# Kernel tuning notes

Hardware: AMD Instinct MI355X
Metric: run time of the kernel (lower is better)

## Reference

```python
import jax, jax.numpy as jnp
import numpy as np

B_GRAPHS = 16
N_PER_GRAPH = 128
N_NODES = B_GRAPHS * N_PER_GRAPH  # 2048
HIDDEN = 256
N_HEADS = 8
HEAD_DIM = HIDDEN // N_HEADS
N_LAYERS = 4
K_RPE = 4
N_EDGES = 32768
NUM_NODE_FEATS = 32
NUM_EDGE_TYPES = 16
MAX_DEGREE = 100
MLP_HID = HIDDEN // 2


def _layernorm(x, s, b):
    m = x.mean(-1, keepdims=True)
    v = jnp.var(x, axis=-1, keepdims=True)
    return (x - m) / jnp.sqrt(v + 1e-5) * s + b


def setup_inputs() -> dict:
    key = jax.random.key(0)
    ks = jax.random.split(key, 24)
    s = 0.02
    x_idx = jax.random.randint(ks[0], (N_NODES,), 0, NUM_NODE_FEATS)
    # edges are intra-graph (the torch code drops cross-graph edges)
    src = jax.random.randint(ks[1], (N_EDGES,), 0, N_NODES)
    dst = (src // N_PER_GRAPH) * N_PER_GRAPH + jax.random.randint(ks[2], (N_EDGES,), 0, N_PER_GRAPH)
    edge_index = jnp.stack([src, dst])
    edge_attr = jax.random.randint(ks[3], (N_EDGES,), 0, NUM_EDGE_TYPES)
    batch = jnp.repeat(jnp.arange(B_GRAPHS), N_PER_GRAPH)
    L = N_LAYERS
    return {
        'x_idx': x_idx, 'edge_index': edge_index, 'edge_attr': edge_attr, 'batch': batch,
        'node_emb': jax.random.normal(ks[4], (NUM_NODE_FEATS, HIDDEN)) * s,
        'edge_emb': jax.random.normal(ks[5], (NUM_EDGE_TYPES, N_HEADS)) * s,
        'degree_emb': jax.random.normal(ks[6], (MAX_DEGREE + 1, HIDDEN)) * s,
        'rpe_W1': jax.random.normal(ks[7], (K_RPE + 1, MLP_HID)) * s,
        'rpe_b1': jnp.zeros((MLP_HID,)),
        'rpe_W2': jax.random.normal(ks[8], (MLP_HID, N_HEADS)) * s,
        'rpe_b2': jnp.zeros((N_HEADS,)),
        'Wq': jax.random.normal(ks[9], (L, HIDDEN, HIDDEN)) * s, 'bq': jnp.zeros((L, HIDDEN)),
        'Wk': jax.random.normal(ks[10], (L, HIDDEN, HIDDEN)) * s, 'bk': jnp.zeros((L, HIDDEN)),
        'Wv': jax.random.normal(ks[11], (L, HIDDEN, HIDDEN)) * s, 'bv': jnp.zeros((L, HIDDEN)),
        'Wo': jax.random.normal(ks[12], (L, HIDDEN, HIDDEN)) * s, 'bo': jnp.zeros((L, HIDDEN)),
        'ln1_s': jnp.ones((L, HIDDEN)), 'ln1_b': jnp.zeros((L, HIDDEN)),
        'ln2_s': jnp.ones((L, HIDDEN)), 'ln2_b': jnp.zeros((L, HIDDEN)),
        'ff_W1': jax.random.normal(ks[13], (L, HIDDEN, 2 * HIDDEN)) * s, 'ff_b1': jnp.zeros((L, 2 * HIDDEN)),
        'ff_W2': jax.random.normal(ks[14], (L, 2 * HIDDEN, HIDDEN)) * s, 'ff_b2': jnp.zeros((L, HIDDEN)),
    }


def _forward(x_idx, edge_index, edge_attr, batch,
             node_emb, edge_emb, degree_emb, rpe_W1, rpe_b1, rpe_W2, rpe_b2,
             Wq, bq, Wk, bk, Wv, bv, Wo, bo, ln1_s, ln1_b, ln2_s, ln2_b,
             ff_W1, ff_b1, ff_W2, ff_b2):
    B, n, H, N = B_GRAPHS, N_PER_GRAPH, N_HEADS, N_NODES
    x = node_emb[x_idx]                               # [N, d]
    src, dst = edge_index[0], edge_index[1]
    # degrees from source endpoints (scatter_add in torch)
    deg = jnp.zeros((N,), jnp.int32).at[src].add(1)
    deg_c = jnp.minimum(deg, MAX_DEGREE)

    # ---- RRWP + edge-type attention bias, block-diagonal over graphs ----
    g = batch[src]
    intra = (batch[src] == batch[dst])                # torch code skips cross-graph edges
    u = src % n
    v = dst % n
    intra_f = intra.astype(jnp.float32)
    inv_du = intra_f / jnp.maximum(deg[src], 1).astype(jnp.float32)
    inv_dv = intra_f / jnp.maximum(deg[dst], 1).astype(jnp.float32)
    # random-walk transition matrix per graph [B, n, n]
    T = (jnp.zeros((B, n, n), jnp.float32)
         .at[g, u, v].add(inv_du)
         .at[g, v, u].add(inv_dv))
    # symmetric edge-type bias per graph [B, n, n, H]
    ev = edge_emb[edge_attr] * intra_f[:, None]
    EB = (jnp.zeros((B, n, n, H), jnp.float32)
          .at[g, u, v].add(ev)
          .at[g, v, u].add(ev))
    # walk powers I, T, T^2, ..., T^K -> [B, n, n, K+1]
    I = jnp.broadcast_to(jnp.eye(n, dtype=jnp.float32), (B, n, n))
    powers = [I, T]
    cur = T
    for _ in range(2, K_RPE + 1):
        cur = cur @ T
        powers.append(cur)
    walk = jnp.stack(powers, axis=-1)
    pair = jax.nn.relu(walk @ rpe_W1 + rpe_b1) @ rpe_W2 + rpe_b2   # [B, n, n, H]
    block = (pair + EB).transpose(0, 3, 1, 2)                      # [B, H, n, n]
    ib = jnp.arange(B)
    full = jnp.full((H, B, n, B, n), -jnp.inf, jnp.float32)
    full = full.at[:, ib, :, ib, :].set(block)                     # diag blocks
    attn_bias = full.reshape(H, N, N)

    # ---- transformer stack ----
    deg_vec = degree_emb[deg_c]
    scale = 1.0 / jnp.sqrt(jnp.float32(HEAD_DIM))
    for l in range(N_LAYERS):
        x = x + deg_vec
        Q = (x @ Wq[l] + bq[l]).reshape(N, H, HEAD_DIM)
        K_ = (x @ Wk[l] + bk[l]).reshape(N, H, HEAD_DIM)
        V = (x @ Wv[l] + bv[l]).reshape(N, H, HEAD_DIM)
        scores = jnp.einsum('ihd,jhd->hij', Q, K_) * scale + attn_bias
        aw = jax.nn.softmax(scores, axis=-1)
        out = jnp.einsum('hij,jhd->ihd', aw, V).reshape(N, HIDDEN)
        out = out @ Wo[l] + bo[l]
        x = _layernorm(x + out, ln1_s[l], ln1_b[l])
        ff = jax.nn.relu(x @ ff_W1[l] + ff_b1[l]) @ ff_W2[l] + ff_b2[l]
        x = _layernorm(x + ff, ln2_s[l], ln2_b[l])
    # global add pool
    return jax.ops.segment_sum(x, batch, num_segments=B)


def reference(x_idx, edge_index, edge_attr, batch,
              node_emb, edge_emb, degree_emb, rpe_W1, rpe_b1, rpe_W2, rpe_b2,
              Wq, bq, Wk, bk, Wv, bv, Wo, bo, ln1_s, ln1_b, ln2_s, ln2_b,
              ff_W1, ff_b1, ff_W2, ff_b2):
    return _forward(x_idx, edge_index, edge_attr, batch,
                    node_emb, edge_emb, degree_emb, rpe_W1, rpe_b1, rpe_W2, rpe_b2,
                    Wq, bq, Wk, bk, Wv, bv, Wo, bo, ln1_s, ln1_b, ln2_s, ln2_b,
                    ff_W1, ff_b1, ff_W2, ff_b2)
```

## Files before the change

kernel.cpp:

```cpp
#include <hip/hip_runtime.h>
#include <hip/hip_bf16.h>

#define B_GRAPHS 16
#define NPG 128
#define NN 2048
#define HIDDEN 256
#define N_HEADS 8
#define HEAD_DIM 32
#define N_LAYERS 4
#define N_EDGES 32768
#define MLP_HID 128
#define MAX_DEG 100

typedef __hip_bfloat16 bf16;
typedef unsigned short ushort_t;
typedef __attribute__((ext_vector_type(8))) short short8;
typedef __attribute__((ext_vector_type(4))) float f32x4;

__device__ __forceinline__ float us2f(ushort_t u) {
    return __uint_as_float(((unsigned)u) << 16);
}
__device__ __forceinline__ ushort_t f2us(float f) {
    unsigned u = __float_as_uint(f);
    return (ushort_t)((u + 0x7FFFu + ((u >> 16) & 1u)) >> 16);
}
__device__ __forceinline__ bool is_bf16_mode(const unsigned* probe) {
    return probe[0] != 0x3F800000u;
}
#define MFMA16(a, b, c) __builtin_amdgcn_mfma_f32_16x16x32_bf16(a, b, c, 0, 0, 0)

__device__ __forceinline__ void gload_lds16(const void* g, void* l) {
    __builtin_amdgcn_global_load_lds(
        (const __attribute__((address_space(1))) unsigned int*)g,
        (__attribute__((address_space(3))) unsigned int*)l, 16, 0, 0);
}
#define SBAR __builtin_amdgcn_s_barrier()
#define WAITPIPE asm volatile("s_waitcnt vmcnt(16) lgkmcnt(0)" ::: "memory")
#define WAITLAST asm volatile("s_waitcnt vmcnt(0) lgkmcnt(0)" ::: "memory")
#define LBAR do { asm volatile("s_waitcnt lgkmcnt(0)" ::: "memory"); SBAR; \
                  asm volatile("" ::: "memory"); } while (0)

#define NW 23
__device__ const int c_wsizes[NW] = {
    8192, 128, 25856, 640, 128, 1024, 8,
    262144, 1024, 262144, 1024, 262144, 1024, 262144, 1024,
    1024, 1024, 1024, 1024,
    524288, 2048, 524288, 1024};
#define TOTW 2144392

#define OFF_NODE_EMB 0
#define OFF_EDGE_EMB 8192
#define OFF_DEG_EMB  8320
#define OFF_RPE_W1   34176
#define OFF_RPE_B1   34816
#define OFF_RPE_W2   34944
#define OFF_RPE_B2   35968
#define OFF_BO       1087624
#define OFF_LN1S     1088648
#define OFF_LN1B     1089672
#define OFF_LN2S     1090696
#define OFF_LN2B     1091720
#define OFF_FFB1     1617032
#define OFF_FFB2     2143368

#define WB_QKV 0
#define WB_O   786432
#define WB_F1  1048576
#define WB_F2  1572864
#define WB_TOT 2097152
#define QKVB_TOT 3072

struct SrcPtrs { const void* p[NW]; };

__global__ void convert_kernel(SrcPtrs sp, const unsigned* __restrict__ probe,
                               float* __restrict__ Wc, float* __restrict__ qkvb) {
    int i = blockIdx.x * 256 + threadIdx.x;
    bool isbf = is_bf16_mode(probe);
    auto rd = [&](int seg, int off) -> float {
        return isbf ? us2f(((const ushort_t*)sp.p[seg])[off])
                    : ((const float*)sp.p[seg])[off];
    };
    if (i < TOTW) {
        int seg = 0, off = i;
        while (seg < NW - 1 && off >= c_wsizes[seg]) { off -= c_wsizes[seg]; seg++; }
        Wc[i] = rd(seg, off);
    } else if (i < TOTW + QKVB_TOT) {
        int j = i - TOTW;
        int l = j / 768, n = j % 768, which = n >> 8, nn = n & 255;
        int seg = (which == 0) ? 8 : (which == 1) ? 10 : 12;
        qkvb[j] = rd(seg, l * 256 + nn);
    }
}

__global__ __launch_bounds__(256) void transpose_pack(SrcPtrs sp,
                                                      const unsigned* __restrict__ probe,
                                                      ushort_t* __restrict__ WB) {
    __shared__ float tile[32][33];
    int b = blockIdx.x;
    bool isbf = is_bf16_mode(probe);
    int seg, soff, srcN, k0, n0, dK;
    size_t doff;
    if (b < 768) {
        int mat = b >> 6, t = b & 63;
        int l = mat / 3, which = mat % 3;
        seg = 7 + which * 2;
        soff = l * 65536; srcN = 256;
        k0 = (t >> 3) * 32; n0 = (t & 7) * 32;
        doff = (size_t)l * 196608 + (size_t)which * 65536; dK = 256;
    } else if (b < 1024) {
        int u = b - 768, l = u >> 6, t = u & 63;
        seg = 13; soff = l * 65536; srcN = 256;
        k0 = (t >> 3) * 32; n0 = (t & 7) * 32;
        doff = WB_O + (size_t)l * 65536; dK = 256;
    } else if (b < 1536) {
        int u = b - 1024, l = u >> 7, t = u & 127;
        seg = 19; soff = l * 131072; srcN = 512;
        k0 = (t >> 4) * 32; n0 = (t & 15) * 32;
        doff = WB_F1 + (size_t)l * 131072; dK = 256;
    } else {
        int u = b - 1536, l = u >> 7, t = u & 127;
        seg = 21; soff = l * 131072; srcN = 256;
        k0 = (t >> 3) * 32; n0 = (t & 7) * 32;
        doff = WB_F2 + (size_t)l * 131072; dK = 512;
    }
    int xcol = threadIdx.x & 31, y8 = threadIdx.x >> 5;
    const void* srcp = sp.p[seg];
#pragma unroll
    for (int rr = 0; rr < 4; rr++) {
        int row = y8 * 4 + rr;
        int off = soff + (k0 + row) * srcN + n0 + xcol;
        tile[row][xcol] = isbf ? us2f(((const ushort_t*)srcp)[off])
                               : ((const float*)srcp)[off];
    }
    __syncthreads();
#pragma unroll
    for (int rr = 0; rr < 4; rr++) {
        int nrow = y8 * 4 + rr;
        WB[doff + (size_t)(n0 + nrow) * dK + k0 + xcol] = f2us(tile[xcol][nrow]);
    }
}

__global__ void zero_kernel(f32x4* __restrict__ p) {
    f32x4 z;
    z[0] = 0.f; z[1] = 0.f; z[2] = 0.f; z[3] = 0.f;
    p[blockIdx.x * 256 + threadIdx.x] = z;
}

__global__ void deg_kernel(const int* __restrict__ src, int* __restrict__ deg) {
    int e = blockIdx.x * blockDim.x + threadIdx.x;
    if (e < N_EDGES) atomicAdd(&deg[src[e]], 1);
}

__global__ void gather_xadd(const int* __restrict__ xidx, const int* __restrict__ deg,
                            const float* __restrict__ emb, const float* __restrict__ demb,
                            float* __restrict__ x, ushort_t* __restrict__ xb) {
    int i = blockIdx.x * blockDim.x + threadIdx.x;
    int node = i >> 8, c = i & 255;
    float v = emb[xidx[node] * HIDDEN + c] + demb[min(deg[node], MAX_DEG) * HIDDEN + c];
    x[i] = v;
    xb[i] = f2us(v);
}

__global__ void scatter_kernel(const int* __restrict__ ei, const int* __restrict__ eattr,
                               const int* __restrict__ batch, const int* __restrict__ deg,
                               const float* __restrict__ edge_emb,
                               float* __restrict__ T, float* __restrict__ bias) {
    int idx = blockIdx.x * blockDim.x + threadIdx.x;
    int e = idx >> 3, h = idx & 7;
    int s = ei[e], d = ei[N_EDGES + e];
    if (batch[s] != batch[d]) return;
    int g = batch[s];
    int u = s & (NPG - 1), v = d & (NPG - 1);
    if (h == 0) {
        atomicAdd(&T[(g * NPG + u) * NPG + v], 1.0f / (float)max(deg[s], 1));
        atomicAdd(&T[(g * NPG + v) * NPG + u], 1.0f / (float)max(deg[d], 1));
    }
    float ev = edge_emb[eattr[e] * N_HEADS + h];
    atomicAdd(&bias[(((size_t)(g * N_HEADS + h) * NPG + u) * NPG + v)], ev);
    atomicAdd(&bias[(((size_t)(g * N_HEADS + h) * NPG + v) * NPG + u)], ev);
}

__global__ void matmul128(const float* __restrict__ A, const float* __restrict__ B,
                          float* __restrict__ C) {
    int g = blockIdx.x / NPG;
    int row = blockIdx.x % NPG;
    int col = threadIdx.x;
    const float* Ag = A + (size_t)g * NPG * NPG;
    const float* Bg = B + (size_t)g * NPG * NPG;
    __shared__ float arow[NPG];
    arow[col] = Ag[row * NPG + col];
    __syncthreads();
    float acc = 0.f;
#pragma unroll 8
    for (int k = 0; k < NPG; k++) acc += arow[k] * Bg[k * NPG + col];
    C[((size_t)g * NPG + row) * NPG + col] = acc;
}

__global__ void matmul128_dual(const float* __restrict__ T2, const float* __restrict__ T,
                               float* __restrict__ T3, float* __restrict__ T4) {
    int half = blockIdx.x >> 11;
    int bid = blockIdx.x & 2047;
    int g = bid / NPG, row = bid % NPG, col = threadIdx.x;
    const float* Ag = T2 + (size_t)g * NPG * NPG;
    const float* Bg = (half ? T2 : T) + (size_t)g * NPG * NPG;
    float* Cg = (half ? T4 : T3) + (size_t)g * NPG * NPG;
    __shared__ float arow[NPG];
    arow[col] = Ag[row * NPG + col];
    __syncthreads();
    float acc = 0.f;
#pragma unroll 8
    for (int k = 0; k < NPG; k++) acc += arow[k] * Bg[k * NPG + col];
    Cg[row * NPG + col] = acc;
}

__global__ __launch_bounds__(256) void rpe_kernel(
    const float* __restrict__ T, const float* __restrict__ T2,
    const float* __restrict__ T3, const float* __restrict__ T4,
    const float* __restrict__ W1, const float* __restrict__ b1,
    const float* __restrict__ W2, const float* __restrict__ b2,
    float* __restrict__ bias) {
    __shared__ float sW1[5][MLP_HID];
    __shared__ float sb1[MLP_HID];
    __shared__ float sW2[MLP_HID][N_HEADS];
    int t = threadIdx.x;
    for (int i = t; i < 5 * MLP_HID; i += 256) sW1[i / MLP_HID][i % MLP_HID] = W1[i];
    for (int i = t; i < MLP_HID; i += 256) sb1[i] = b1[i];
    for (int i = t; i < MLP_HID * N_HEADS; i += 256) sW2[i / N_HEADS][i % N_HEADS] = W2[i];
    __syncthreads();
    int p = blockIdx.x * 256 + t;
    int g = p / (NPG * NPG);
    int rem = p % (NPG * NPG);
    int i = rem / NPG, j = rem % NPG;
    float f0 = (i == j) ? 1.f : 0.f;
    float f1 = T[p], f2 = T2[p], f3 = T3[p], f4 = T4[p];
    float acc[N_HEADS];
#pragma unroll
    for (int h = 0; h < N_HEADS; h++) acc[h] = b2[h];
#pragma unroll 4
    for (int m = 0; m < MLP_HID; m++) {
        float hv = sb1[m] + f0 * sW1[0][m] + f1 * sW1[1][m] + f2 * sW1[2][m] +
                   f3 * sW1[3][m] + f4 * sW1[4][m];
        hv = fmaxf(hv, 0.f);
#pragma unroll
        for (int h = 0; h < N_HEADS; h++) acc[h] += hv * sW2[m][h];
    }
#pragma unroll
    for (int h = 0; h < N_HEADS; h++)
        bias[(((size_t)(g * N_HEADS + h) * NPG + i) * NPG + j)] += acc[h];
}

__global__ __launch_bounds__(256, 1) void qkv_attn(
    const ushort_t* __restrict__ x_bf, const ushort_t* __restrict__ WT,
    const float* __restrict__ qb, const float* __restrict__ bias,
    ushort_t* __restrict__ ao) {
    int bid = blockIdx.x;
    int g = bid >> 4, h = (bid >> 1) & 7, half = bid & 1;
    int wave = threadIdx.x >> 6, lane = threadIdx.x & 63;
    int lr = lane & 15, lq = lane >> 4;

    __shared__ char Wbuf[3][16384];
    __shared__ ushort_t Qs[64][40];
    __shared__ ushort_t Ks[NPG][40];
    __shared__ ushort_t VT[32][136];
    __shared__ ushort_t P[4][16][136];

    const ushort_t* xg = x_bf + (size_t)g * NPG * HIDDEN;
    int qrow = half * 64 + wave * 16;
    int kvrow = wave * 32;

    short8 Aq[8], Akv[2][8];
#pragma unroll
    for (int kk = 0; kk < 8; kk++) {
        Aq[kk] = *(const short8*)(xg + (size_t)(qrow + lr) * 256 + kk * 32 + lq * 8);
#pragma unroll
        for (int i = 0; i < 2; i++)
            Akv[i][kk] = *(const short8*)(xg + (size_t)(kvrow + i * 16 + lr) * 256 +
                                          kk * 32 + lq * 8);
    }
    float bqv[2], bkv[2], bvv[2];
#pragma unroll
    for (int j = 0; j < 2; j++) {
        int c = h * 32 + j * 16 + lr;
        bqv[j] = qb[c]; bkv[j] = qb[256 + c]; bvv[j] = qb[512 + c];
    }
    asm volatile("s_waitcnt vmcnt(0) lgkmcnt(0)" ::: "memory");

    auto stageW = [&](int rowbase, int c) {
        const char* gW = (const char*)WT;
        char* lb = &Wbuf[c][0] + wave * 4096;
#pragma unroll
        for (int it = 0; it < 4; it++) {
            int j = wave * 4096 + it * 1024 + lane * 16;
            int n = j >> 9, off = j & 511;
            gload_lds16(gW + (size_t)(rowbase + n) * 512 + (off ^ ((n & 7) << 4)),
                        lb + it * 1024);
        }
        __builtin_amdgcn_sched_barrier(0);
    };
    stageW(h * 32, 0);
    stageW(256 + h * 32, 1);
    stageW(512 + h * 32, 2);

    const float* bg = bias + (size_t)(g * N_HEADS + h) * NPG * NPG;
    float bgv[8][4];
#pragma unroll
    for (int r = 0; r < 4; r++) {
        int i = half * 64 + wave * 16 + lq * 4 + r;
#pragma unroll
        for (int jt = 0; jt < 8; jt++)
            bgv[jt][r] = bg[(size_t)i * NPG + jt * 16 + lr];
    }
    __builtin_amdgcn_sched_barrier(0);

    auto rdW = [&](int c, int jt, int kk) -> short8 {
        int n = jt * 16 + lr;
        int off = n * 512 + ((kk * 64 + lq * 16) ^ ((n & 7) << 4));
        return *(const short8*)(&Wbuf[c][off]);
    };

    f32x4 qa[2]{}, ka[2][2]{}, va[2][2]{};
    asm volatile("s_waitcnt vmcnt(40)" ::: "memory"); SBAR;
#pragma unroll
    for (int kk = 0; kk < 8; kk++)
#pragma unroll
        for (int j = 0; j < 2; j++)
            qa[j] = MFMA16(Aq[kk], rdW(0, j, kk), qa[j]);

    asm volatile("s_waitcnt vmcnt(36)" ::: "memory"); SBAR;
#pragma unroll
    for (int kk = 0; kk < 8; kk++)
#pragma unroll
        for (int j = 0; j < 2; j++)
#pragma unroll
            for (int i = 0; i < 2; i++)
                ka[i][j] = MFMA16(Akv[i][kk], rdW(1, j, kk), ka[i][j]);

    asm volatile("s_waitcnt vmcnt(32)" ::: "memory"); SBAR;
#pragma unroll
    for (int kk = 0; kk < 8; kk++)
#pragma unroll
        for (int j = 0; j < 2; j++)
#pragma unroll
            for (int i = 0; i < 2; i++)
                va[i][j] = MFMA16(Akv[i][kk], rdW(2, j, kk), va[i][j]);

#pragma unroll
    for (int j = 0; j < 2; j++) {
        int c = j * 16 + lr;
#pragma unroll
        for (int r = 0; r < 4; r++) {
            Qs[wave * 16 + lq * 4 + r][c] = f2us(qa[j][r] + bqv[j]);
#pragma unroll
            for (int i = 0; i < 2; i++) {
                int row = kvrow + i * 16 + lq * 4 + r;
                Ks[row][c] = f2us(ka[i][j][r] + bkv[j]);
                VT[c][row] = f2us(va[i][j][r] + bvv[j]);
            }
        }
    }
    __syncthreads();

    short8 qf = *(const short8*)(&Qs[wave * 16 + lr][lq * 8]);
    f32x4 S[8];
    f32x4 zero;
    zero[0] = 0.f; zero[1] = 0.f; zero[2] = 0.f; zero[3] = 0.f;
#pragma unroll
    for (int jt = 0; jt < 8; jt++) {
        short8 kf = *(const short8*)(&Ks[jt * 16 + lr][lq * 8]);
        S[jt] = MFMA16(qf, kf, zero);
    }

    const float scale = 0.17677669529663687f;
    float lrow[4];
#pragma unroll
    for (int r = 0; r < 4; r++) {
        float mx = -1e30f;
#pragma unroll
        for (int jt = 0; jt < 8; jt++) {
            float s = S[jt][r] * scale + bgv[jt][r];
            S[jt][r] = s;
            mx = fmaxf(mx, s);
        }
#pragma unroll
        for (int m = 1; m < 16; m <<= 1) mx = fmaxf(mx, __shfl_xor(mx, m));
        float sum = 0.f;
#pragma unroll
        for (int jt = 0; jt < 8; jt++) {
            float e = __expf(S[jt][r] - mx);
            S[jt][r] = e;
            sum += e;
        }
#pragma unroll
        for (int m = 1; m < 16; m <<= 1) sum += __shfl_xor(sum, m);
        lrow[r] = sum;
    }

#pragma unroll
    for (int jt = 0; jt < 8; jt++)
#pragma unroll
        for (int r = 0; r < 4; r++)
            P[wave][lq * 4 + r][jt * 16 + lr] = f2us(S[jt][r]);

    f32x4 O[2]{};
#pragma unroll
    for (int k0 = 0; k0 < NPG; k0 += 32) {
        short8 pa = *(const short8*)(&P[wave][lr][k0 + lq * 8]);
#pragma unroll
        for (int dt = 0; dt < 2; dt++) {
            short8 vb = *(const short8*)(&VT[dt * 16 + lr][k0 + lq * 8]);
            O[dt] = MFMA16(pa, vb, O[dt]);
        }
    }
#pragma unroll
    for (int r = 0; r < 4; r++) {
        float inv = 1.f / lrow[r];
        int row = g * NPG + half * 64 + wave * 16 + lq * 4 + r;
#pragma unroll
        for (int dt = 0; dt < 2; dt++)
            ao[(size_t)row * HIDDEN + h * 32 + dt * 16 + lr] = f2us(O[dt][r] * inv);
    }
}

__global__ __launch_bounds__(256, 1) void fused_mlp(
    const ushort_t* __restrict__ ao, const ushort_t* __restrict__ WoT,
    const float* __restrict__ bo, const float* __restrict__ ln1s,
    const float* __restrict__ ln1b,
    const ushort_t* __restrict__ F1T, const ushort_t* __restrict__ F2T,
    const float* __restrict__ fb1, const float* __restrict__ fb2,
    const float* __restrict__ ln2s, const float* __restrict__ ln2b,
    const float* __restrict__ xin, const int* __restrict__ deg,
    const float* __restrict__ demb, int add_deg,
    float* __restrict__ xout, ushort_t* __restrict__ xb) {
    int m0 = blockIdx.x * 8;
    int wave = threadIdx.x >> 6, lane = threadIdx.x & 63;
    int lr = lane & 15, lq = lane >> 4;
    int ar = m0 + (lr & 7);

    __shared__ ushort_t Wbuf[2][32768];
    __shared__ ushort_t xs_bf[8][264];
    __shared__ ushort_t ffh[8][520];
    __shared__ float ws[4][16], qs[4][16];

    auto stageO = [&](int h, int b) {
        const char* gW = (const char*)WoT;
        char* lb = (char*)&Wbuf[b][0] + wave * 16384;
#pragma unroll
        for (int it = 0; it < 16; it++) {
            int j = wave * 16384 + it * 1024 + lane * 16;
            int n = j >> 8, off = j & 255;
            gload_lds16(gW + n * 512 + h * 256 + (off ^ ((n & 7) << 4)), lb + it * 1024);
        }
        __builtin_amdgcn_sched_barrier(0);
    };
    auto stageF1 = [&](int q, int b) {
        const char* gW = (const char*)F1T;
        char* lb = (char*)&Wbuf[b][0] + wave * 16384;
#pragma unroll
        for (int it = 0; it < 16; it++) {
            int j = wave * 16384 + it * 1024 + lane * 16;
            int n = j >> 9, off = j & 511;
            gload_lds16(gW + (q * 128 + n) * 512 + (off ^ ((n & 7) << 4)), lb + it * 1024);
        }
        __builtin_amdgcn_sched_barrier(0);
    };
    auto stageF2 = [&](int q, int b) {
        const char* gW = (const char*)F2T;
        char* lb = (char*)&Wbuf[b][0] + wave * 16384;
#pragma unroll
        for (int it = 0; it < 16; it++) {
            int j = wave * 16384 + it * 1024 + lane * 16;
            int n = j >> 8, off = j & 255;
            gload_lds16(gW + n * 1024 + q * 256 + (off ^ ((n & 7) << 4)), lb + it * 1024);
        }
        __builtin_amdgcn_sched_barrier(0);
    };

    float bo_v[4], l1s[4], l1b[4], fb2v[4], l2s[4], l2b[4], xres[4][4], fb1q[4][2];
#pragma unroll
    for (int jt = 0; jt < 4; jt++) {
        int col = wave * 64 + jt * 16 + lr;
        bo_v[jt] = bo[col]; l1s[jt] = ln1s[col]; l1b[jt] = ln1b[col];
        fb2v[jt] = fb2[col]; l2s[jt] = ln2s[col]; l2b[jt] = ln2b[col];
#pragma unroll
        for (int r = 0; r < 4; r++) {
            int row = m0 + ((lq * 4 + r) & 7);
            xres[jt][r] = xin[(size_t)row * 256 + col];
        }
    }
#pragma unroll
    for (int q = 0; q < 4; q++)
#pragma unroll
        for (int t = 0; t < 2; t++)
            fb1q[q][t] = fb1[q * 128 + wave * 32 + t * 16 + lr];
    int dg4[4];
    if (add_deg) {
#pragma unroll
        for (int r = 0; r < 4; r++)
            dg4[r] = min(deg[m0 + ((lq * 4 + r) & 7)], MAX_DEG);
    }
    short8 Af[8];
#pragma unroll
    for (int t = 0; t < 8; t++)
        Af[t] = *(const short8*)(ao + (size_t)ar * 256 + t * 32 + lq * 8);

    stageO(0, 0);
    stageO(1, 1);

    f32x4 acc[4]{};
#pragma unroll
    for (int h = 0; h < 2; h++) {
        WAITPIPE; SBAR; asm volatile("" ::: "memory");
#pragma unroll
        for (int kk = 0; kk < 4; kk++) {
            short8 a = Af[h * 4 + kk];
#pragma unroll
            for (int jt = 0; jt < 4; jt++) {
                int n = wave * 64 + jt * 16 + lr;
                int bo_ = n * 256 + ((kk * 64 + lq * 16) ^ ((n & 7) << 4));
                short8 bf = *(const short8*)((const char*)&Wbuf[h][0] + bo_);
                acc[jt] = MFMA16(a, bf, acc[jt]);
            }
        }
        LBAR;
        if (h == 0) stageF1(0, 0);
        else        stageF1(1, 1);
    }

    float valLN[4][4], meanst[4];
#pragma unroll
    for (int r = 0; r < 4; r++) {
        float s = 0.f;
#pragma unroll
        for (int jt = 0; jt < 4; jt++) {
            float v = acc[jt][r] + bo_v[jt] + xres[jt][r];
            valLN[jt][r] = v;
            s += v;
        }
#pragma unroll
        for (int m = 1; m < 16; m <<= 1) s += __shfl_xor(s, m);
        if (lr == 0) ws[wave][lq * 4 + r] = s;
    }
    LBAR;
#pragma unroll
    for (int r = 0; r < 4; r++) {
        int rr = lq * 4 + r;
        float mean = (ws[0][rr] + ws[1][rr] + ws[2][rr] + ws[3][rr]) * (1.f / 256.f);
        meanst[r] = mean;
        float q = 0.f;
#pragma unroll
        for (int jt = 0; jt < 4; jt++) {
            float d = valLN[jt][r] - mean;
            q += d * d;
        }
#pragma unroll
        for (int m = 1; m < 16; m <<= 1) q += __shfl_xor(q, m);
        if (lr == 0) qs[wave][rr] = q;
    }
    LBAR;
#pragma unroll
    for (int r = 0; r < 4; r++) {
        int rr = lq * 4 + r;
        float var = (qs[0][rr] + qs[1][rr] + qs[2][rr] + qs[3][rr]) * (1.f / 256.f);
        float rstd = rsqrtf(var + 1e-5f);
#pragma unroll
        for (int jt = 0; jt < 4; jt++) {
            int col = wave * 64 + jt * 16 + lr;
            float y = (valLN[jt][r] - meanst[r]) * rstd * l1s[jt] + l1b[jt];
            valLN[jt][r] = y;
            if (rr < 8) xs_bf[rr][col] = f2us(y);
        }
    }

#pragma unroll
    for (int q = 0; q < 4; q++) {
        WAITPIPE; SBAR; asm volatile("" ::: "memory");
        f32x4 a1[2]{};
#pragma unroll
        for (int kk = 0; kk < 8; kk++) {
            short8 a = *(const short8*)(&xs_bf[lr & 7][kk * 32 + lq * 8]);
#pragma unroll
            for (int t = 0; t < 2; t++) {
                int n = wave * 32 + t * 16 + lr;
                int bo_ = n * 512 + ((kk * 64 + lq * 16) ^ ((n & 7) << 4));
                short8 bf = *(const short8*)((const char*)&Wbuf[q & 1][0] + bo_);
                a1[t] = MFMA16(a, bf, a1[t]);
            }
        }
#pragma unroll
        for (int t = 0; t < 2; t++) {
            int col = q * 128 + wave * 32 + t * 16 + lr;
#pragma unroll
            for (int r = 0; r < 4; r++) {
                int rr = lq * 4 + r;
                if (rr < 8) ffh[rr][col] = f2us(fmaxf(a1[t][r] + fb1q[q][t], 0.f));
            }
        }
        LBAR;
        if (q < 2) stageF1(q + 2, q & 1);
        else       stageF2(q - 2, q & 1);
    }

    f32x4 acc2[4]{};
#pragma unroll
    for (int q = 0; q < 4; q++) {
        if (q == 3) { WAITLAST; } else { WAITPIPE; }
        SBAR; asm volatile("" ::: "memory");
#pragma unroll
        for (int kk = 0; kk < 4; kk++) {
            short8 a = *(const short8*)(&ffh[lr & 7][q * 128 + kk * 32 + lq * 8]);
#pragma unroll
            for (int jt = 0; jt < 4; jt++) {
                int n = wave * 64 + jt * 16 + lr;
                int bo_ = n * 256 + ((kk * 64 + lq * 16) ^ ((n & 7) << 4));
                short8 bf = *(const short8*)((const char*)&Wbuf[q & 1][0] + bo_);
                acc2[jt] = MFMA16(a, bf, acc2[jt]);
            }
        }
        LBAR;
        if (q < 2) stageF2(q + 2, q & 1);
    }

    float val2[4][4];
#pragma unroll
    for (int r = 0; r < 4; r++) {
        int rr = lq * 4 + r;
        float s = 0.f;
#pragma unroll
        for (int jt = 0; jt < 4; jt++) {
            float v = acc2[jt][r] + fb2v[jt] + valLN[jt][r];
            val2[jt][r] = v;
            s += v;
        }
#pragma unroll
        for (int m = 1; m < 16; m <<= 1) s += __shfl_xor(s, m);
        if (lr == 0) ws[wave][rr] = s;
    }
    __syncthreads();
#pragma unroll
    for (int r = 0; r < 4; r++) {
        int rr = lq * 4 + r;
        float mean = (ws[0][rr] + ws[1][rr] + ws[2][rr] + ws[3][rr]) * (1.f / 256.f);
        meanst[r] = mean;
        float q = 0.f;
#pragma unroll
        for (int jt = 0; jt < 4; jt++) {
            float d = val2[jt][r] - mean;
            q += d * d;
        }
#pragma unroll
        for (int m = 1; m < 16; m <<= 1) q += __shfl_xor(q, m);
        if (lr == 0) qs[wave][rr] = q;
    }
    __syncthreads();
#pragma unroll
    for (int r = 0; r < 4; r++) {
        int rr = lq * 4 + r;
        float var = (qs[0][rr] + qs[1][rr] + qs[2][rr] + qs[3][rr]) * (1.f / 256.f);
        float rstd = rsqrtf(var + 1e-5f);
        if (rr < 8) {
            int row = m0 + rr;
#pragma unroll
            for (int jt = 0; jt < 4; jt++) {
                int col = wave * 64 + jt * 16 + lr;
                float y = (val2[jt][r] - meanst[r]) * rstd * l2s[jt] + l2b[jt];
                if (add_deg) y += demb[dg4[r] * 256 + col];
                xout[(size_t)row * 256 + col] = y;
                xb[(size_t)row * 256 + col] = f2us(y);
            }
        }
    }
}

__global__ void pool_kernel(const float* __restrict__ x, void* __restrict__ out,
                            const unsigned* __restrict__ probe) {
    int b = blockIdx.x;
    int c = threadIdx.x;
    float acc = 0.f;
#pragma unroll 4
    for (int i = 0; i < NPG; i++) acc += x[(size_t)(b * NPG + i) * HIDDEN + c];
    if (is_bf16_mode(probe))
        ((bf16*)out)[b * HIDDEN + c] = __float2bfloat16(acc);
    else
        ((float*)out)[b * HIDDEN + c] = acc;
}

extern "C" void kernel_launch(void* const* d_in, const int* in_sizes, int n_in,
                              void* d_out, int out_size, void* d_ws, size_t ws_size,
                              hipStream_t stream) {
    const int* x_idx      = (const int*)d_in[0];
    const int* edge_index = (const int*)d_in[1];
    const int* edge_attr  = (const int*)d_in[2];
    const int* batch      = (const int*)d_in[3];
    const unsigned* probe = (const unsigned*)d_in[19];

    char* base = (char*)d_ws;
    float* Wc    = (float*)base;       base += (size_t)TOTW * 4;
    float* x     = (float*)base;       base += (size_t)NN * HIDDEN * 4;
    float* T     = (float*)base;       base += 262144 * 4;
    float* bias  = (float*)base;       base += (size_t)2097152 * 4;
    int*   deg   = (int*)base;         base += 2048 * 4;
    float* T2    = (float*)base;       base += 262144 * 4;
    float* T3    = (float*)base;       base += 262144 * 4;
    float* T4    = (float*)base;       base += 262144 * 4;
    float* qkvb  = (float*)base;       base += QKVB_TOT * 4;
    ushort_t* WB    = (ushort_t*)base; base += (size_t)WB_TOT * 2;
    ushort_t* x_bf  = (ushort_t*)base; base += (size_t)NN * HIDDEN * 2;
    ushort_t* ao_bf = (ushort_t*)base; base += (size_t)NN * HIDDEN * 2;

    SrcPtrs sp;
    for (int i = 0; i < NW; i++) sp.p[i] = d_in[4 + i];

    zero_kernel<<<2306, 256, 0, stream>>>((f32x4*)T);
    convert_kernel<<<(TOTW + QKVB_TOT + 255) / 256, 256, 0, stream>>>(sp, probe, Wc, qkvb);
    transpose_pack<<<2048, 256, 0, stream>>>(sp, probe, WB);
    deg_kernel<<<N_EDGES / 256, 256, 0, stream>>>(edge_index, deg);
    gather_xadd<<<NN, 256, 0, stream>>>(x_idx, deg, Wc + OFF_NODE_EMB, Wc + OFF_DEG_EMB,
                                        x, x_bf);
    scatter_kernel<<<N_EDGES * 8 / 256, 256, 0, stream>>>(edge_index, edge_attr, batch, deg,
                                                          Wc + OFF_EDGE_EMB, T, bias);
    matmul128<<<B_GRAPHS * NPG, NPG, 0, stream>>>(T, T, T2);
    matmul128_dual<<<2 * B_GRAPHS * NPG, NPG, 0, stream>>>(T2, T, T3, T4);
    rpe_kernel<<<(B_GRAPHS * NPG * NPG) / 256, 256, 0, stream>>>(
        T, T2, T3, T4, Wc + OFF_RPE_W1, Wc + OFF_RPE_B1, Wc + OFF_RPE_W2, Wc + OFF_RPE_B2,
        bias);

    for (int l = 0; l < N_LAYERS; l++) {
        qkv_attn<<<2 * B_GRAPHS * N_HEADS, 256, 0, stream>>>(
            x_bf, WB + WB_QKV + (size_t)l * 196608, qkvb + l * 768, bias, ao_bf);
        fused_mlp<<<NN / 8, 256, 0, stream>>>(
            ao_bf, WB + WB_O + (size_t)l * 65536, Wc + OFF_BO + l * 256,
            Wc + OFF_LN1S + l * 256, Wc + OFF_LN1B + l * 256,
            WB + WB_F1 + (size_t)l * 131072, WB + WB_F2 + (size_t)l * 131072,
            Wc + OFF_FFB1 + l * 512, Wc + OFF_FFB2 + l * 256,
            Wc + OFF_LN2S + l * 256, Wc + OFF_LN2B + l * 256, x,
            deg, Wc + OFF_DEG_EMB, (l < N_LAYERS - 1) ? 1 : 0, x, x_bf);
    }
    pool_kernel<<<B_GRAPHS, 256, 0, stream>>>(x, d_out, probe);
}
```

Baseline: 343.4 us.

## Merge prep kernels and widen fused MLP to eight waves per block

The zero, convert and transpose kernels become one launch, and the gather and scatter kernels become a second, cutting launch count in the setup phase. The fused MLP block grows from 256 to 512 threads (8 waves). Each wave now owns half as many output columns and stages half as much weight data per buffer, and the wait count is adjusted to match. This spreads the per-block MFMA and staging work over more waves to improve latency hiding. In exchange the LayerNorm reductions must sum across 8 partials, and the block carries more waves and barrier overhead.

```diff
diff --git a/kernel.cpp b/kernel.cpp
--- a/kernel.cpp
+++ b/kernel.cpp
@@ -35,7 +35,7 @@
         (__attribute__((address_space(3))) unsigned int*)l, 16, 0, 0);
 }
 #define SBAR __builtin_amdgcn_s_barrier()
-#define WAITPIPE asm volatile("s_waitcnt vmcnt(16) lgkmcnt(0)" ::: "memory")
+#define WAITP8 asm volatile("s_waitcnt vmcnt(8) lgkmcnt(0)" ::: "memory")
 #define WAITLAST asm volatile("s_waitcnt vmcnt(0) lgkmcnt(0)" ::: "memory")
 #define LBAR do { asm volatile("s_waitcnt lgkmcnt(0)" ::: "memory"); SBAR; \
                   asm volatile("" ::: "memory"); } while (0)
@@ -70,80 +70,82 @@
 #define WB_TOT 2097152
 #define QKVB_TOT 3072
 
+#define ZERO_BLKS 2306
+#define CONV_BLKS 8389
+#define TP_BLKS   2048
+
 struct SrcPtrs { const void* p[NW]; };
 
-__global__ void convert_kernel(SrcPtrs sp, const unsigned* __restrict__ probe,
-                               float* __restrict__ Wc, float* __restrict__ qkvb) {
-    int i = blockIdx.x * 256 + threadIdx.x;
+__global__ __launch_bounds__(256) void prep1(SrcPtrs sp, const unsigned* __restrict__ probe,
+                                             float* __restrict__ Wc, float* __restrict__ qkvb,
+                                             f32x4* __restrict__ zerop,
+                                             ushort_t* __restrict__ WB) {
+    __shared__ float tile[32][33];
+    int b = blockIdx.x;
     bool isbf = is_bf16_mode(probe);
     auto rd = [&](int seg, int off) -> float {
         return isbf ? us2f(((const ushort_t*)sp.p[seg])[off])
                     : ((const float*)sp.p[seg])[off];
     };
-    if (i < TOTW) {
-        int seg = 0, off = i;
-        while (seg < NW - 1 && off >= c_wsizes[seg]) { off -= c_wsizes[seg]; seg++; }
-        Wc[i] = rd(seg, off);
-    } else if (i < TOTW + QKVB_TOT) {
-        int j = i - TOTW;
-        int l = j / 768, n = j % 768, which = n >> 8, nn = n & 255;
-        int seg = (which == 0) ? 8 : (which == 1) ? 10 : 12;
-        qkvb[j] = rd(seg, l * 256 + nn);
-    }
-}
-
-__global__ __launch_bounds__(256) void transpose_pack(SrcPtrs sp,
-                                                      const unsigned* __restrict__ probe,
-                                                      ushort_t* __restrict__ WB) {
-    __shared__ float tile[32][33];
-    int b = blockIdx.x;
-    bool isbf = is_bf16_mode(probe);
-    int seg, soff, srcN, k0, n0, dK;
-    size_t doff;
-    if (b < 768) {
-        int mat = b >> 6, t = b & 63;
-        int l = mat / 3, which = mat % 3;
-        seg = 7 + which * 2;
-        soff = l * 65536; srcN = 256;
-        k0 = (t >> 3) * 32; n0 = (t & 7) * 32;
-        doff = (size_t)l * 196608 + (size_t)which * 65536; dK = 256;
-    } else if (b < 1024) {
-        int u = b - 768, l = u >> 6, t = u & 63;
-        seg = 13; soff = l * 65536; srcN = 256;
-        k0 = (t >> 3) * 32; n0 = (t & 7) * 32;
-        doff = WB_O + (size_t)l * 65536; dK = 256;
-    } else if (b < 1536) {
-        int u = b - 1024, l = u >> 7, t = u & 127;
-        seg = 19; soff = l * 131072; srcN = 512;
-        k0 = (t >> 4) * 32; n0 = (t & 15) * 32;
-        doff = WB_F1 + (size_t)l * 131072; dK = 256;
+    if (b < ZERO_BLKS) {
+        f32x4 z;
+        z[0] = 0.f; z[1] = 0.f; z[2] = 0.f; z[3] = 0.f;
+        zerop[b * 256 + threadIdx.x] = z;
+    } else if (b < ZERO_BLKS + CONV_BLKS) {
+        int i = (b - ZERO_BLKS) * 256 + threadIdx.x;
+        if (i < TOTW) {
+            int seg = 0, off = i;
+            while (seg < NW - 1 && off >= c_wsizes[seg]) { off -= c_wsizes[seg]; seg++; }
+            Wc[i] = rd(seg, off);
+        } else if (i < TOTW + QKVB_TOT) {
+            int j = i - TOTW;
+            int l = j / 768, n = j % 768, which = n >> 8, nn = n & 255;
+            int seg = (which == 0) ? 8 : (which == 1) ? 10 : 12;
+            qkvb[j] = rd(seg, l * 256 + nn);
+        }
     } else {
-        int u = b - 1536, l = u >> 7, t = u & 127;
-        seg = 21; soff = l * 131072; srcN = 256;
-        k0 = (t >> 3) * 32; n0 = (t & 7) * 32;
-        doff = WB_F2 + (size_t)l * 131072; dK = 512;
-    }
-    int xcol = threadIdx.x & 31, y8 = threadIdx.x >> 5;
-    const void* srcp = sp.p[seg];
-#pragma unroll
-    for (int rr = 0; rr < 4; rr++) {
-        int row = y8 * 4 + rr;
-        int off = soff + (k0 + row) * srcN + n0 + xcol;
-        tile[row][xcol] = isbf ? us2f(((const ushort_t*)srcp)[off])
-                               : ((const float*)srcp)[off];
-    }
-    __syncthreads();
-#pragma unroll
-    for (int rr = 0; rr < 4; rr++) {
-        int nrow = y8 * 4 + rr;
-        WB[doff + (size_t)(n0 + nrow) * dK + k0 + xcol] = f2us(tile[xcol][nrow]);
-    }
-}
-
-__global__ void zero_kernel(f32x4* __restrict__ p) {
-    f32x4 z;
-    z[0] = 0.f; z[1] = 0.f; z[2] = 0.f; z[3] = 0.f;
-    p[blockIdx.x * 256 + threadIdx.x] = z;
+        int tb = b - ZERO_BLKS - CONV_BLKS;
+        int seg, soff, srcN, k0, n0, dK;
+        size_t doff;
+        if (tb < 768) {
+            int mat = tb >> 6, t = tb & 63;
+            int l = mat / 3, which = mat % 3;
+            seg = 7 + which * 2;
+            soff = l * 65536; srcN = 256;
+            k0 = (t >> 3) * 32; n0 = (t & 7) * 32;
+            doff = (size_t)l * 196608 + (size_t)which * 65536; dK = 256;
+        } else if (tb < 1024) {
+            int u = tb - 768, l = u >> 6, t = u & 63;
+            seg = 13; soff = l * 65536; srcN = 256;
+            k0 = (t >> 3) * 32; n0 = (t & 7) * 32;
+            doff = WB_O + (size_t)l * 65536; dK = 256;
+        } else if (tb < 1536) {
+            int u = tb - 1024, l = u >> 7, t = u & 127;
+            seg = 19; soff = l * 131072; srcN = 512;
+            k0 = (t >> 4) * 32; n0 = (t & 15) * 32;
+            doff = WB_F1 + (size_t)l * 131072; dK = 256;
+        } else {
+            int u = tb - 1536, l = u >> 7, t = u & 127;
+            seg = 21; soff = l * 131072; srcN = 256;
+            k0 = (t >> 3) * 32; n0 = (t & 7) * 32;
+            doff = WB_F2 + (size_t)l * 131072; dK = 512;
+        }
+        int xcol = threadIdx.x & 31, y8 = threadIdx.x >> 5;
+        const void* srcp = sp.p[seg];
+#pragma unroll
+        for (int rr = 0; rr < 4; rr++) {
+            int row = y8 * 4 + rr;
+            int off = soff + (k0 + row) * srcN + n0 + xcol;
+            tile[row][xcol] = isbf ? us2f(((const ushort_t*)srcp)[off])
+                                   : ((const float*)srcp)[off];
+        }
+        __syncthreads();
+#pragma unroll
+        for (int rr = 0; rr < 4; rr++) {
+            int nrow = y8 * 4 + rr;
+            WB[doff + (size_t)(n0 + nrow) * dK + k0 + xcol] = f2us(tile[xcol][nrow]);
+        }
+    }
 }
 
 __global__ void deg_kernel(const int* __restrict__ src, int* __restrict__ deg) {
@@ -151,33 +153,34 @@
     if (e < N_EDGES) atomicAdd(&deg[src[e]], 1);
 }
 
-__global__ void gather_xadd(const int* __restrict__ xidx, const int* __restrict__ deg,
-                            const float* __restrict__ emb, const float* __restrict__ demb,
-                            float* __restrict__ x, ushort_t* __restrict__ xb) {
-    int i = blockIdx.x * blockDim.x + threadIdx.x;
-    int node = i >> 8, c = i & 255;
-    float v = emb[xidx[node] * HIDDEN + c] + demb[min(deg[node], MAX_DEG) * HIDDEN + c];
-    x[i] = v;
-    xb[i] = f2us(v);
-}
-
-__global__ void scatter_kernel(const int* __restrict__ ei, const int* __restrict__ eattr,
-                               const int* __restrict__ batch, const int* __restrict__ deg,
-                               const float* __restrict__ edge_emb,
-                               float* __restrict__ T, float* __restrict__ bias) {
-    int idx = blockIdx.x * blockDim.x + threadIdx.x;
-    int e = idx >> 3, h = idx & 7;
-    int s = ei[e], d = ei[N_EDGES + e];
-    if (batch[s] != batch[d]) return;
-    int g = batch[s];
-    int u = s & (NPG - 1), v = d & (NPG - 1);
-    if (h == 0) {
-        atomicAdd(&T[(g * NPG + u) * NPG + v], 1.0f / (float)max(deg[s], 1));
-        atomicAdd(&T[(g * NPG + v) * NPG + u], 1.0f / (float)max(deg[d], 1));
-    }
-    float ev = edge_emb[eattr[e] * N_HEADS + h];
-    atomicAdd(&bias[(((size_t)(g * N_HEADS + h) * NPG + u) * NPG + v)], ev);
-    atomicAdd(&bias[(((size_t)(g * N_HEADS + h) * NPG + v) * NPG + u)], ev);
+__global__ void prep2(const int* __restrict__ xidx, const int* __restrict__ deg,
+                      const float* __restrict__ emb, const float* __restrict__ demb,
+                      float* __restrict__ x, ushort_t* __restrict__ xb,
+                      const int* __restrict__ ei, const int* __restrict__ eattr,
+                      const int* __restrict__ batch, const float* __restrict__ edge_emb,
+                      float* __restrict__ T, float* __restrict__ bias) {
+    int b = blockIdx.x;
+    if (b < 2048) {
+        int i = b * 256 + threadIdx.x;
+        int node = i >> 8, c = i & 255;
+        float v = emb[xidx[node] * HIDDEN + c] + demb[min(deg[node], MAX_DEG) * HIDDEN + c];
+        x[i] = v;
+        xb[i] = f2us(v);
+    } else {
+        int idx = (b - 2048) * 256 + threadIdx.x;
+        int e = idx >> 3, h = idx & 7;
+        int s = ei[e], d = ei[N_EDGES + e];
+        if (batch[s] != batch[d]) return;
+        int g = batch[s];
+        int u = s & (NPG - 1), v = d & (NPG - 1);
+        if (h == 0) {
+            atomicAdd(&T[(g * NPG + u) * NPG + v], 1.0f / (float)max(deg[s], 1));
+            atomicAdd(&T[(g * NPG + v) * NPG + u], 1.0f / (float)max(deg[d], 1));
+        }
+        float ev = edge_emb[eattr[e] * N_HEADS + h];
+        atomicAdd(&bias[(((size_t)(g * N_HEADS + h) * NPG + u) * NPG + v)], ev);
+        atomicAdd(&bias[(((size_t)(g * N_HEADS + h) * NPG + v) * NPG + u)], ev);
+    }
 }
 
 __global__ void matmul128(const float* __restrict__ A, const float* __restrict__ B,
@@ -421,7 +424,7 @@
     }
 }
 
-__global__ __launch_bounds__(256, 1) void fused_mlp(
+__global__ __launch_bounds__(512, 2) void fused_mlp(
     const ushort_t* __restrict__ ao, const ushort_t* __restrict__ WoT,
     const float* __restrict__ bo, const float* __restrict__ ln1s,
     const float* __restrict__ ln1b,
@@ -439,14 +442,14 @@
     __shared__ ushort_t Wbuf[2][32768];
     __shared__ ushort_t xs_bf[8][264];
     __shared__ ushort_t ffh[8][520];
-    __shared__ float ws[4][16], qs[4][16];
+    __shared__ float ws[8][16], qs[8][16];
 
     auto stageO = [&](int h, int b) {
         const char* gW = (const char*)WoT;
-        char* lb = (char*)&Wbuf[b][0] + wave * 16384;
-#pragma unroll
-        for (int it = 0; it < 16; it++) {
-            int j = wave * 16384 + it * 1024 + lane * 16;
+        char* lb = (char*)&Wbuf[b][0] + wave * 8192;
+#pragma unroll
+        for (int it = 0; it < 8; it++) {
+            int j = wave * 8192 + it * 1024 + lane * 16;
             int n = j >> 8, off = j & 255;
             gload_lds16(gW + n * 512 + h * 256 + (off ^ ((n & 7) << 4)), lb + it * 1024);
         }
@@ -454,10 +457,10 @@
     };
     auto stageF1 = [&](int q, int b) {
         const char* gW = (const char*)F1T;
-        char* lb = (char*)&Wbuf[b][0] + wave * 16384;
-#pragma unroll
-        for (int it = 0; it < 16; it++) {
-            int j = wave * 16384 + it * 1024 + lane * 16;
+        char* lb = (char*)&Wbuf[b][0] + wave * 8192;
+#pragma unroll
+        for (int it = 0; it < 8; it++) {
+            int j = wave * 8192 + it * 1024 + lane * 16;
             int n = j >> 9, off = j & 511;
             gload_lds16(gW + (q * 128 + n) * 512 + (off ^ ((n & 7) << 4)), lb + it * 1024);
         }
@@ -465,20 +468,20 @@
     };
     auto stageF2 = [&](int q, int b) {
         const char* gW = (const char*)F2T;
-        char* lb = (char*)&Wbuf[b][0] + wave * 16384;
-#pragma unroll
-        for (int it = 0; it < 16; it++) {
-            int j = wave * 16384 + it * 1024 + lane * 16;
+        char* lb = (char*)&Wbuf[b][0] + wave * 8192;
+#pragma unroll
+        for (int it = 0; it < 8; it++) {
+            int j = wave * 8192 + it * 1024 + lane * 16;
             int n = j >> 8, off = j & 255;
             gload_lds16(gW + n * 1024 + q * 256 + (off ^ ((n & 7) << 4)), lb + it * 1024);
         }
         __builtin_amdgcn_sched_barrier(0);
     };
 
-    float bo_v[4], l1s[4], l1b[4], fb2v[4], l2s[4], l2b[4], xres[4][4], fb1q[4][2];
-#pragma unroll
-    for (int jt = 0; jt < 4; jt++) {
-        int col = wave * 64 + jt * 16 + lr;
+    float bo_v[2], l1s[2], l1b[2], fb2v[2], l2s[2], l2b[2], xres[2][4], fb1q[4];
+#pragma unroll
+    for (int jt = 0; jt < 2; jt++) {
+        int col = wave * 32 + jt * 16 + lr;
         bo_v[jt] = bo[col]; l1s[jt] = ln1s[col]; l1b[jt] = ln1b[col];
         fb2v[jt] = fb2[col]; l2s[jt] = ln2s[col]; l2b[jt] = ln2b[col];
 #pragma unroll
@@ -488,10 +491,7 @@
         }
     }
 #pragma unroll
-    for (int q = 0; q < 4; q++)
-#pragma unroll
-        for (int t = 0; t < 2; t++)
-            fb1q[q][t] = fb1[q * 128 + wave * 32 + t * 16 + lr];
+    for (int q = 0; q < 4; q++) fb1q[q] = fb1[q * 128 + wave * 16 + lr];
     int dg4[4];
     if (add_deg) {
 #pragma unroll
@@ -506,16 +506,16 @@
     stageO(0, 0);
     stageO(1, 1);
 
-    f32x4 acc[4]{};
+    f32x4 acc[2]{};
 #pragma unroll
     for (int h = 0; h < 2; h++) {
-        WAITPIPE; SBAR; asm volatile("" ::: "memory");
+        WAITP8; SBAR; asm volatile("" ::: "memory");
 #pragma unroll
         for (int kk = 0; kk < 4; kk++) {
             short8 a = Af[h * 4 + kk];
 #pragma unroll
-            for (int jt = 0; jt < 4; jt++) {
-                int n = wave * 64 + jt * 16 + lr;
+            for (int jt = 0; jt < 2; jt++) {
+                int n = wave * 32 + jt * 16 + lr;
                 int bo_ = n * 256 + ((kk * 64 + lq * 16) ^ ((n & 7) << 4));
                 short8 bf = *(const short8*)((const char*)&Wbuf[h][0] + bo_);
                 acc[jt] = MFMA16(a, bf, acc[jt]);
@@ -526,12 +526,12 @@
         else        stageF1(1, 1);
     }
 
-    float valLN[4][4], meanst[4];
+    float valLN[2][4], meanst[4];
 #pragma unroll
     for (int r = 0; r < 4; r++) {
         float s = 0.f;
 #pragma unroll
-        for (int jt = 0; jt < 4; jt++) {
+        for (int jt = 0; jt < 2; jt++) {
             float v = acc[jt][r] + bo_v[jt] + xres[jt][r];
             valLN[jt][r] = v;
             s += v;
@@ -544,11 +544,14 @@
 #pragma unroll
     for (int r = 0; r < 4; r++) {
         int rr = lq * 4 + r;
-        float mean = (ws[0][rr] + ws[1][rr] + ws[2][rr] + ws[3][rr]) * (1.f / 256.f);
+        float sum = 0.f;
+#pragma unroll
+        for (int c = 0; c < 8; c++) sum += ws[c][rr];
+        float mean = sum * (1.f / 256.f);
         meanst[r] = mean;
         float q = 0.f;
 #pragma unroll
-        for (int jt = 0; jt < 4; jt++) {
+        for (int jt = 0; jt < 2; jt++) {
             float d = valLN[jt][r] - mean;
             q += d * d;
         }
@@ -560,11 +563,13 @@
 #pragma unroll
     for (int r = 0; r < 4; r++) {
         int rr = lq * 4 + r;
-        float var = (qs[0][rr] + qs[1][rr] + qs[2][rr] + qs[3][rr]) * (1.f / 256.f);
-        float rstd = rsqrtf(var + 1e-5f);
-#pragma unroll
-        for (int jt = 0; jt < 4; jt++) {
-            int col = wave * 64 + jt * 16 + lr;
+        float qsum = 0.f;
+#pragma unroll
+        for (int c = 0; c < 8; c++) qsum += qs[c][rr];
+        float rstd = rsqrtf(qsum * (1.f / 256.f) + 1e-5f);
+#pragma unroll
+        for (int jt = 0; jt < 2; jt++) {
+            int col = wave * 32 + jt * 16 + lr;
             float y = (valLN[jt][r] - meanst[r]) * rstd * l1s[jt] + l1b[jt];
             valLN[jt][r] = y;
             if (rr < 8) xs_bf[rr][col] = f2us(y);
@@ -573,44 +578,38 @@
 
 #pragma unroll
     for (int q = 0; q < 4; q++) {
-        WAITPIPE; SBAR; asm volatile("" ::: "memory");
-        f32x4 a1[2]{};
+        WAITP8; SBAR; asm volatile("" ::: "memory");
+        f32x4 a1{};
+        int nl = wave * 16 + lr;
 #pragma unroll
         for (int kk = 0; kk < 8; kk++) {
             short8 a = *(const short8*)(&xs_bf[lr & 7][kk * 32 + lq * 8]);
-#pragma unroll
-            for (int t = 0; t < 2; t++) {
-                int n = wave * 32 + t * 16 + lr;
-                int bo_ = n * 512 + ((kk * 64 + lq * 16) ^ ((n & 7) << 4));
-                short8 bf = *(const short8*)((const char*)&Wbuf[q & 1][0] + bo_);
-                a1[t] = MFMA16(a, bf, a1[t]);
-            }
-        }
-#pragma unroll
-        for (int t = 0; t < 2; t++) {
-            int col = q * 128 + wave * 32 + t * 16 + lr;
-#pragma unroll
-            for (int r = 0; r < 4; r++) {
-                int rr = lq * 4 + r;
-                if (rr < 8) ffh[rr][col] = f2us(fmaxf(a1[t][r] + fb1q[q][t], 0.f));
-            }
+            int bo_ = nl * 512 + ((kk * 64 + lq * 16) ^ ((nl & 7) << 4));
+            short8 bf = *(const short8*)((const char*)&Wbuf[q & 1][0] + bo_);
+            a1 = MFMA16(a, bf, a1);
+        }
+        int col = q * 128 + wave * 16 + lr;
+#pragma unroll
+        for (int r = 0; r < 4; r++) {
+            int rr = lq * 4 + r;
+            if (rr < 8) ffh[rr][col] = f2us(fmaxf(a1[r] + fb1q[q], 0.f));
         }
         LBAR;
         if (q < 2) stageF1(q + 2, q & 1);
         else       stageF2(q - 2, q & 1);
     }
 
-    f32x4 acc2[4]{};
+    f32x4 acc2[2]{};
 #pragma unroll
     for (int q = 0; q < 4; q++) {
-        if (q == 3) { WAITLAST; } else { WAITPIPE; }
+        if (q == 3) { WAITLAST; } else { WAITP8; }
         SBAR; asm volatile("" ::: "memory");
 #pragma unroll
         for (int kk = 0; kk < 4; kk++) {
             short8 a = *(const short8*)(&ffh[lr & 7][q * 128 + kk * 32 + lq * 8]);
 #pragma unroll
-            for (int jt = 0; jt < 4; jt++) {
-                int n = wave * 64 + jt * 16 + lr;
+            for (int jt = 0; jt < 2; jt++) {
+                int n = wave * 32 + jt * 16 + lr;
                 int bo_ = n * 256 + ((kk * 64 + lq * 16) ^ ((n & 7) << 4));
                 short8 bf = *(const short8*)((const char*)&Wbuf[q & 1][0] + bo_);
                 acc2[jt] = MFMA16(a, bf, acc2[jt]);
@@ -620,13 +619,13 @@
         if (q < 2) stageF2(q + 2, q & 1);
     }
 
-    float val2[4][4];
+    float val2[2][4];
 #pragma unroll
     for (int r = 0; r < 4; r++) {
         int rr = lq * 4 + r;
         float s = 0.f;
 #pragma unroll
-        for (int jt = 0; jt < 4; jt++) {
+        for (int jt = 0; jt < 2; jt++) {
             float v = acc2[jt][r] + fb2v[jt] + valLN[jt][r];
             val2[jt][r] = v;
             s += v;
@@ -639,11 +638,14 @@
 #pragma unroll
     for (int r = 0; r < 4; r++) {
         int rr = lq * 4 + r;
-        float mean = (ws[0][rr] + ws[1][rr] + ws[2][rr] + ws[3][rr]) * (1.f / 256.f);
+        float sum = 0.f;
+#pragma unroll
+        for (int c = 0; c < 8; c++) sum += ws[c][rr];
+        float mean = sum * (1.f / 256.f);
         meanst[r] = mean;
         float q = 0.f;
 #pragma unroll
-        for (int jt = 0; jt < 4; jt++) {
+        for (int jt = 0; jt < 2; jt++) {
             float d = val2[jt][r] - mean;
             q += d * d;
         }
@@ -655,13 +657,15 @@
 #pragma unroll
     for (int r = 0; r < 4; r++) {
         int rr = lq * 4 + r;
-        float var = (qs[0][rr] + qs[1][rr] + qs[2][rr] + qs[3][rr]) * (1.f / 256.f);
-        float rstd = rsqrtf(var + 1e-5f);
+        float qsum = 0.f;
+#pragma unroll
+        for (int c = 0; c < 8; c++) qsum += qs[c][rr];
+        float rstd = rsqrtf(qsum * (1.f / 256.f) + 1e-5f);
         if (rr < 8) {
             int row = m0 + rr;
 #pragma unroll
-            for (int jt = 0; jt < 4; jt++) {
-                int col = wave * 64 + jt * 16 + lr;
+            for (int jt = 0; jt < 2; jt++) {
+                int col = wave * 32 + jt * 16 + lr;
                 float y = (val2[jt][r] - meanst[r]) * rstd * l2s[jt] + l2b[jt];
                 if (add_deg) y += demb[dg4[r] * 256 + col];
                 xout[(size_t)row * 256 + col] = y;
@@ -710,14 +714,12 @@
     SrcPtrs sp;
     for (int i = 0; i < NW; i++) sp.p[i] = d_in[4 + i];
 
-    zero_kernel<<<2306, 256, 0, stream>>>((f32x4*)T);
-    convert_kernel<<<(TOTW + QKVB_TOT + 255) / 256, 256, 0, stream>>>(sp, probe, Wc, qkvb);
-    transpose_pack<<<2048, 256, 0, stream>>>(sp, probe, WB);
+    prep1<<<ZERO_BLKS + CONV_BLKS + TP_BLKS, 256, 0, stream>>>(sp, probe, Wc, qkvb,
+                                                               (f32x4*)T, WB);
     deg_kernel<<<N_EDGES / 256, 256, 0, stream>>>(edge_index, deg);
-    gather_xadd<<<NN, 256, 0, stream>>>(x_idx, deg, Wc + OFF_NODE_EMB, Wc + OFF_DEG_EMB,
-                                        x, x_bf);
-    scatter_kernel<<<N_EDGES * 8 / 256, 256, 0, stream>>>(edge_index, edge_attr, batch, deg,
-                                                          Wc + OFF_EDGE_EMB, T, bias);
+    prep2<<<3072, 256, 0, stream>>>(x_idx, deg, Wc + OFF_NODE_EMB, Wc + OFF_DEG_EMB,
+                                    x, x_bf, edge_index, edge_attr, batch,
+                                    Wc + OFF_EDGE_EMB, T, bias);
     matmul128<<<B_GRAPHS * NPG, NPG, 0, stream>>>(T, T, T2);
     matmul128_dual<<<2 * B_GRAPHS * NPG, NPG, 0, stream>>>(T2, T, T3, T4);
     rpe_kernel<<<(B_GRAPHS * NPG * NPG) / 256, 256, 0, stream>>>(
@@ -727,7 +729,7 @@
     for (int l = 0; l < N_LAYERS; l++) {
         qkv_attn<<<2 * B_GRAPHS * N_HEADS, 256, 0, stream>>>(
             x_bf, WB + WB_QKV + (size_t)l * 196608, qkvb + l * 768, bias, ao_bf);
-        fused_mlp<<<NN / 8, 256, 0, stream>>>(
+        fused_mlp<<<NN / 8, 512, 0, stream>>>(
             ao_bf, WB + WB_O + (size_t)l * 65536, Wc + OFF_BO + l * 256,
             Wc + OFF_LN1S + l * 256, Wc + OFF_LN1B + l * 256,
             WB + WB_F1 + (size_t)l * 131072, WB + WB_F2 + (size_t)l * 131072,
```

Result: faster. 331.9 us (-3.3%).
